# Optimization experiments

Measured on AMD Instinct MI355X. Metric: run time of the kernel, lower is better.

## Reference

```python
import jax, jax.numpy as jnp
import numpy as np
import math

B, S, D = 4, 1024, 1024
H, DK = 16, 64
NUM_BUCKETS, MAX_DIST = 32, 128


def _relative_position_bucket(relative_position, num_buckets=NUM_BUCKETS, max_distance=MAX_DIST):
    # bidirectional bucketing (T5 encoder style)
    num_buckets = num_buckets // 2
    buckets = (relative_position > 0).astype(jnp.int32) * num_buckets
    rp = jnp.abs(relative_position)
    max_exact = num_buckets // 2
    is_small = rp < max_exact
    # clamp to >=1 to avoid log(0); masked out by is_small anyway
    rp_large = max_exact + (
        jnp.log(jnp.maximum(rp, 1).astype(jnp.float32) / max_exact)
        / math.log(max_distance / max_exact)
        * (num_buckets - max_exact)
    ).astype(jnp.int32)
    rp_large = jnp.minimum(rp_large, num_buckets - 1)
    return buckets + jnp.where(is_small, rp, rp_large)


def compute_bias(rel_bias_table, q_len, k_len):
    ctx = jnp.arange(q_len)[:, None]
    mem = jnp.arange(k_len)[None, :]
    buckets = _relative_position_bucket(mem - ctx)  # [q,k]
    values = rel_bias_table[buckets]  # [q,k,H]
    return jnp.transpose(values, (2, 0, 1))  # [H,q,k]


def setup_inputs() -> dict:
    key = jax.random.key(0)
    ks = jax.random.split(key, 6)
    return {
        "hidden_states": jax.random.normal(ks[0], (B, S, D), dtype=jnp.float32),
        "Wq": jax.random.normal(ks[1], (D, H * DK), dtype=jnp.float32) * 0.02,
        "Wk": jax.random.normal(ks[2], (D, H * DK), dtype=jnp.float32) * 0.02,
        "Wv": jax.random.normal(ks[3], (D, H * DK), dtype=jnp.float32) * 0.02,
        "Wo": jax.random.normal(ks[4], (H * DK, D), dtype=jnp.float32) * 0.02,
        "rel_bias_table": jax.random.normal(ks[5], (NUM_BUCKETS, H), dtype=jnp.float32),
    }


def reference(hidden_states, Wq, Wk, Wv, Wo, rel_bias_table):
    b, s, _ = hidden_states.shape
    # projections (no bias), split heads -> [b,h,s,dk]
    def heads(x):
        return jnp.transpose(x.reshape(b, s, H, DK), (0, 2, 1, 3))
    q = heads(hidden_states @ Wq)
    k = heads(hidden_states @ Wk)
    v = heads(hidden_states @ Wv)
    # NOTE: T5 attention is UNSCALED (no 1/sqrt(dk))
    scores = jnp.einsum("bhqd,bhkd->bhqk", q, k)
    bias = compute_bias(rel_bias_table, s, s)[None]  # [1,H,s,s]
    scores = scores + bias
    attn = jax.nn.softmax(scores.astype(jnp.float32), axis=-1).astype(scores.dtype)
    out = jnp.einsum("bhqk,bhkd->bhqd", attn, v)
    out = jnp.transpose(out, (0, 2, 1, 3)).reshape(b, s, H * DK)
    return out @ Wo
```

## Files before the change

### kernel.cpp

```cpp
#include <hip/hip_runtime.h>
#include <hip/hip_bf16.h>

typedef __attribute__((ext_vector_type(8))) short short8;
typedef __attribute__((ext_vector_type(4))) float f32x4;
typedef __attribute__((ext_vector_type(4))) unsigned u32x4;
typedef unsigned short u16;

#define AS1 __attribute__((address_space(1)))
#define AS3 __attribute__((address_space(3)))

#define LOG2E 1.44269504088896f
#define FOLD_M 46.166241308446828f
#define EXP2(x) __builtin_amdgcn_exp2f(x)
#define WAITV(n) asm volatile("s_waitcnt vmcnt(" #n ")" ::: "memory")

__device__ __forceinline__ u16 f2bf(float f) {
    unsigned u = __builtin_bit_cast(unsigned, f);
    u += 0x7FFFu + ((u >> 16) & 1u);
    return (u16)(u >> 16);
}

__device__ __forceinline__ unsigned pk2(float a, float b) {
    unsigned ua = __builtin_bit_cast(unsigned, a) + 0x8000u;
    unsigned ub = __builtin_bit_cast(unsigned, b) + 0x8000u;
    return __builtin_amdgcn_perm(ub, ua, 0x07060302);
}

__global__ __launch_bounds__(256) void k_prep(const float* __restrict__ hidden,
                                              const float* __restrict__ Wq, const float* __restrict__ Wk,
                                              const float* __restrict__ Wv, const float* __restrict__ Wo,
                                              const float* __restrict__ tbl,
                                              u16* __restrict__ hidb,
                                              u16* __restrict__ wt, u16* __restrict__ wot,
                                              float* __restrict__ bias2) {
    int z = blockIdx.z;
    if (z >= 5) {
        int i = ((z - 5) * 1024 + blockIdx.y * 32 + blockIdx.x) * 256 + threadIdx.x;
        float4 v = ((const float4*)hidden)[i];
        ushort4 o;
        o.x = f2bf(v.x); o.y = f2bf(v.y); o.z = f2bf(v.z); o.w = f2bf(v.w);
        ((ushort4*)hidb)[i] = o;
        return;
    }
    if (z == 4) {
        int idx = (blockIdx.y * 32 + blockIdx.x) * 256 + threadIdx.x;
        if (idx < 16 * 2048) {
            int r = idx & 2047, h = idx >> 11;
            int rel = r - 1023;
            int bucket = rel > 0 ? 16 : 0;
            int rp = rel < 0 ? -rel : rel;
            if (rp < 8) bucket += rp;
            else {
                int lb = 8 + (int)(log2f((float)rp * 0.125f) * 2.0f);
                bucket += (lb < 15 ? lb : 15);
            }
            bias2[idx] = tbl[bucket * 16 + h] * LOG2E - FOLD_M;
        }
        return;
    }
    const float* in = z == 0 ? Wq : z == 1 ? Wk : z == 2 ? Wv : Wo;
    u16* out = (z == 3) ? wot : wt + (size_t)z * 1024 * 1024;
    __shared__ float tile[32][33];
    int tx = threadIdx.x & 31, ty = threadIdx.x >> 5;
    int bx = blockIdx.x << 5, by = blockIdx.y << 5;
    #pragma unroll
    for (int j = 0; j < 32; j += 8)
        tile[ty + j][tx] = in[(size_t)(by + ty + j) * 1024 + bx + tx];
    __syncthreads();
    #pragma unroll
    for (int j = 0; j < 32; j += 8)
        out[(size_t)(bx + ty + j) * 1024 + by + tx] = f2bf(tile[tx][ty + j]);
}

__global__ __launch_bounds__(512, 2) void k_qkv(const u16* __restrict__ A, const u16* __restrict__ Bt,
                                                u16* __restrict__ oq, u16* __restrict__ ok,
                                                u16* __restrict__ ov) {
    __shared__ __align__(16) u16 As[2][256 * 64];
    __shared__ __align__(16) u16 Bs[2][192 * 64];
    int t = threadIdx.x, lane = t & 63, wave = t >> 6;
    int g = lane >> 4, ln = lane & 15;
    int wr = wave >> 2, wc = wave & 3;

    int bid = blockIdx.x;
    int xcd = bid & 7, wgl = bid >> 3;
    int mt = ((xcd & 3) << 2) + (wgl >> 3);
    int nt = ((xcd >> 2) << 3) + (wgl & 7);
    int m0 = mt << 8, n0 = nt * 192;

    f32x4 acc[8][3];
    #pragma unroll
    for (int i = 0; i < 8; i++)
        #pragma unroll
        for (int j = 0; j < 3; j++) acc[i][j] = (f32x4){0.f, 0.f, 0.f, 0.f};

    #define QSTG(kt_, buf_)                                                                      \
        {                                                                                        \
            _Pragma("unroll")                                                                    \
            for (int u = 0; u < 4; u++) {                                                        \
                int L = t * 16 + u * 8192;                                                       \
                int row = L >> 7, gI = (L >> 4) & 7, gp = gI ^ (row & 7);                        \
                __builtin_amdgcn_global_load_lds(                                                \
                    (const AS1 void*)(A + (size_t)(m0 + row) * 1024 + (kt_) * 64 + gp * 8),      \
                    (AS3 void*)&As[buf_][L >> 1], 16, 0, 0);                                     \
            }                                                                                    \
            _Pragma("unroll")                                                                    \
            for (int u = 0; u < 3; u++) {                                                        \
                int L = t * 16 + u * 8192;                                                       \
                int row = L >> 7, gI = (L >> 4) & 7, gp = gI ^ (row & 7);                        \
                __builtin_amdgcn_global_load_lds(                                                \
                    (const AS1 void*)(Bt + (size_t)(n0 + row) * 1024 + (kt_) * 64 + gp * 8),     \
                    (AS3 void*)&Bs[buf_][L >> 1], 16, 0, 0);                                     \
            }                                                                                    \
        }

    QSTG(0, 0);
    __syncthreads();

    #pragma unroll 2
    for (int kt = 0; kt < 16; kt++) {
        const int c = kt & 1;
        if (kt < 15) QSTG(kt + 1, c ^ 1);

        #pragma unroll
        for (int ks = 0; ks < 2; ks++) {
            short8 af[8], bfr[3];
            int cb = ((ks << 2) + g) << 4;
            #pragma unroll
            for (int mf = 0; mf < 8; mf++) {
                int row = (wr << 7) + (mf << 4) + ln;
                af[mf] = *(const short8*)((const char*)&As[c][0] + row * 128 + (cb ^ ((row & 7) << 4)));
            }
            #pragma unroll
            for (int nf = 0; nf < 3; nf++) {
                int row = wc * 48 + (nf << 4) + ln;
                bfr[nf] = *(const short8*)((const char*)&Bs[c][0] + row * 128 + (cb ^ ((row & 7) << 4)));
            }
            __builtin_amdgcn_s_setprio(1);
            #pragma unroll
            for (int mf = 0; mf < 8; mf++)
                #pragma unroll
                for (int nf = 0; nf < 3; nf++)
                    acc[mf][nf] = __builtin_amdgcn_mfma_f32_16x16x32_bf16(af[mf], bfr[nf], acc[mf][nf], 0, 0, 0);
            __builtin_amdgcn_s_setprio(0);
        }
        __syncthreads();
    }
    #undef QSTG

    #pragma unroll
    for (int mf = 0; mf < 8; mf++)
        #pragma unroll
        for (int nf = 0; nf < 3; nf++) {
            int mb = m0 + (wr << 7) + (mf << 4) + (g << 2);
            int n = n0 + wc * 48 + (nf << 4) + ln;
            int j = n >> 10, col = n & 1023;
            int h = col >> 6, dk = col & 63;
            int b = mb >> 10, s = mb & 1023;
            if (j == 2) {
                ushort4 pk;
                pk.x = f2bf(acc[mf][nf][0]); pk.y = f2bf(acc[mf][nf][1]);
                pk.z = f2bf(acc[mf][nf][2]); pk.w = f2bf(acc[mf][nf][3]);
                *(ushort4*)(ov + ((size_t)(((b << 4) + h) * 64 + dk)) * 1024 + s) = pk;
            } else {
                u16* dst = (j == 0) ? oq : ok;
                #pragma unroll
                for (int r = 0; r < 4; r++)
                    dst[((size_t)(((b << 4) + h) * 1024 + s + r)) * 64 + dk] = f2bf(acc[mf][nf][r]);
            }
        }
}

__global__ __launch_bounds__(256) void k_gemm_out(const u16* __restrict__ A, const u16* __restrict__ Bt,
                                                  float* __restrict__ outf) {
    const int K = 1024, N = 1024;
    __shared__ __align__(16) u16 As[3][2048];
    __shared__ __align__(16) u16 Bs[3][4096];
    int t = threadIdx.x, lane = t & 63, wave = t >> 6;
    int bid = blockIdx.y * 8 + blockIdx.x;
    int sbid = (bid & 7) * 64 + (bid >> 3);
    int m0 = (sbid / 8) * 64, n0 = (sbid % 8) << 7;
    int wm = (wave >> 1) * 32, wn = (wave & 1) << 6;
    int g = lane >> 4, ln = lane & 15;
    f32x4 acc[2][4];
    #pragma unroll
    for (int i = 0; i < 2; i++)
        #pragma unroll
        for (int j = 0; j < 4; j++) acc[i][j] = (f32x4){0.f, 0.f, 0.f, 0.f};

    int schunk = ((lane & 3) ^ ((lane >> 3) & 3)) << 3;
    const u16* gA = A + (size_t)(m0 + wave * 16 + (lane >> 2)) * K + schunk;
    const u16* gB = Bt + (size_t)(n0 + wave * 16 + (lane >> 2)) * K + schunk;
    int ldsOff = wave * 512;

    #define GSTAGE(k0_, buf_)                                                                          \
        {                                                                                              \
            u16* sA = &As[buf_][0];                                                                    \
            u16* sB = &Bs[buf_][0];                                                                    \
            __builtin_amdgcn_global_load_lds((const AS1 void*)(gA + (k0_)),                            \
                                             (AS3 void*)&sA[ldsOff], 16, 0, 0);                        \
            __builtin_amdgcn_global_load_lds((const AS1 void*)(gB + (k0_)),                            \
                                             (AS3 void*)&sB[ldsOff], 16, 0, 0);                        \
            __builtin_amdgcn_global_load_lds((const AS1 void*)(gB + 64 * K + (k0_)),                   \
                                             (AS3 void*)&sB[ldsOff + 2048], 16, 0, 0);                 \
        }

    GSTAGE(0, 0);
    GSTAGE(32, 1);

    int rchunk = (g ^ ((ln >> 1) & 3)) << 3;
    int c0 = 0, c2 = 2;

    for (int kb = 0; kb < 32; kb++) {
        if (kb < 30) {
            GSTAGE((kb + 2) * 32, c2);
            WAITV(6);
        } else if (kb == 30) {
            WAITV(3);
        } else {
            WAITV(0);
        }
        __builtin_amdgcn_s_barrier();

        const u16* rA = &As[c0][0];
        const u16* rB = &Bs[c0][0];
        short8 af[2], bfr[4];
        #pragma unroll
        for (int fm = 0; fm < 2; fm++)
            af[fm] = *(const short8*)&rA[(wm + (fm << 4) + ln) * 32 + rchunk];
        #pragma unroll
        for (int fn = 0; fn < 4; fn++)
            bfr[fn] = *(const short8*)&rB[(wn + (fn << 4) + ln) * 32 + rchunk];
        __builtin_amdgcn_s_setprio(1);
        #pragma unroll
        for (int fm = 0; fm < 2; fm++)
            #pragma unroll
            for (int fn = 0; fn < 4; fn++)
                acc[fm][fn] = __builtin_amdgcn_mfma_f32_16x16x32_bf16(af[fm], bfr[fn], acc[fm][fn], 0, 0, 0);
        __builtin_amdgcn_s_setprio(0);
        __builtin_amdgcn_s_barrier();

        int old = c0;
        c0 = (c0 == 2) ? 0 : c0 + 1;
        c2 = old;
    }

    #pragma unroll
    for (int fm = 0; fm < 2; fm++)
        #pragma unroll
        for (int fn = 0; fn < 4; fn++) {
            int mb = m0 + wm + (fm << 4) + (g << 2);
            int n = n0 + wn + (fn << 4) + ln;
            #pragma unroll
            for (int r = 0; r < 4; r++)
                outf[(size_t)(mb + r) * N + n] = acc[fm][fn][r];
        }
    #undef GSTAGE
}

__global__ __launch_bounds__(256, 2) void k_attn(const u16* __restrict__ Qg, const u16* __restrict__ Kg,
                                                 const u16* __restrict__ Vtg, const float* __restrict__ bias2,
                                                 u16* __restrict__ attn_out) {
    __shared__ __align__(16) u16 Ks[2][64 * 64];
    __shared__ __align__(16) u16 Vts[2][64 * 64];
    __shared__ __align__(16) float blds4[4][1160];

    int t = threadIdx.x, lane = t & 63, w = t >> 6;
    int bid = blockIdx.x;
    int sid = (bid & 7) * 64 + (bid >> 3);
    int qb = sid & 7, h = (sid >> 3) & 15, b = sid >> 7;
    int q0 = qb << 7;
    const u16* Qh = Qg + ((size_t)(((b << 4) + h) * 1024 + q0)) * 64;
    const u16* Kh = Kg + (size_t)(((b << 4) + h)) * 1024 * 64;
    const u16* Vth = Vtg + (size_t)(((b << 4) + h)) * 64 * 1024;
    const float* bh = bias2 + (h << 11);

    int g = lane >> 4, ln = lane & 15;
    int lnk = (ln & 3) | ((ln & 4) << 1) | ((ln & 8) >> 1);
    int kbq = ((g & 1) << 3) | ((g >> 1) << 2);

    short8 qf[2][2];
    #pragma unroll
    for (int fm = 0; fm < 2; fm++)
        #pragma unroll
        for (int kh = 0; kh < 2; kh++)
            qf[fm][kh] = *(const short8*)(Qh + (size_t)(w * 32 + fm * 16 + ln) * 64 + kh * 32 + g * 8);

    int w0 = 896 - q0;
    for (int i = t; i < 1152; i += 256) {
        float v = bh[w0 + i];
        #pragma unroll
        for (int a2 = 0; a2 < 4; a2++) { int x = i - a2; if (x >= 0) blds4[a2][x] = v; }
    }
    float b_hi = bh[1023 + 256];
    float b_lo = bh[1023 - 256];
    int aRep = (3 - ln) & 3;
    const float* repB = &blds4[aRep][0];

    #define STAGE(kb_, buf_)                                                                     \
        {                                                                                        \
            _Pragma("unroll")                                                                    \
            for (int r2 = 0; r2 < 2; r2++) {                                                     \
                int L = t * 16 + r2 * 4096;                                                      \
                int row = L >> 7, gI = (L >> 4) & 7, gp = gI ^ (row & 7);                        \
                __builtin_amdgcn_global_load_lds(                                                \
                    (const AS1 void*)(Kh + (size_t)((kb_) * 64 + row) * 64 + gp * 8),            \
                    (AS3 void*)&Ks[buf_][L >> 1], 16, 0, 0);                                     \
                __builtin_amdgcn_global_load_lds(                                                \
                    (const AS1 void*)(Vth + (size_t)row * 1024 + (kb_) * 64 + gp * 8),           \
                    (AS3 void*)&Vts[buf_][L >> 1], 16, 0, 0);                                    \
            }                                                                                    \
        }

    STAGE(0, 0);
    __syncthreads();

    float psum[2] = {0.f, 0.f};
    f32x4 o[2][4];
    #pragma unroll
    for (int fm = 0; fm < 2; fm++)
        #pragma unroll
        for (int dn = 0; dn < 4; dn++) o[fm][dn] = (f32x4){0.f, 0.f, 0.f, 0.f};

    #pragma unroll 2
    for (int kb = 0; kb < 16; kb++) {
        const int cur = kb & 1;
        if (kb < 15) STAGE(kb + 1, cur ^ 1);

        f32x4 s[2][4];
        __builtin_amdgcn_s_setprio(1);
        #pragma unroll
        for (int fn = 0; fn < 4; fn++) {
            int row = (fn << 4) + lnk;
            short8 kf0 = *(const short8*)((const char*)Ks[cur] + row * 128 + (((g << 4) + 0)  ^ ((row & 7) << 4)));
            short8 kf1 = *(const short8*)((const char*)Ks[cur] + row * 128 + (((g << 4) + 64) ^ ((row & 7) << 4)));
            #pragma unroll
            for (int fm = 0; fm < 2; fm++) {
                f32x4 a = (f32x4){0.f, 0.f, 0.f, 0.f};
                a = __builtin_amdgcn_mfma_f32_16x16x32_bf16(kf0, qf[fm][0], a, 0, 0, 0);
                a = __builtin_amdgcn_mfma_f32_16x16x32_bf16(kf1, qf[fm][1], a, 0, 0, 0);
                s[fm][fn] = a;
            }
        }
        __builtin_amdgcn_s_setprio(0);

        int d0 = 64 * kb - q0 - 32 * w;
        int ibase = 64 * kb - 32 * w + 127 + kbq - ln;
        bool fast = (d0 >= 122) || (d0 <= -154);
        float bu = d0 > 0 ? b_hi : b_lo;
        unsigned Px[2][4], Py[2][4];
        #pragma unroll
        for (int fm = 0; fm < 2; fm++)
            #pragma unroll
            for (int fn = 0; fn < 4; fn++) {
                f32x4 sv = s[fm][fn];
                float b0, b1, b2v, b3;
                if (fast) { b0 = b1 = b2v = b3 = bu; }
                else {
                    float4 bb = *(const float4*)(repB + (ibase + 16 * fn - 16 * fm - aRep));
                    b0 = bb.x; b1 = bb.y; b2v = bb.z; b3 = bb.w;
                }
                float p0 = EXP2(fmaf(sv[0], LOG2E, b0));
                float p1 = EXP2(fmaf(sv[1], LOG2E, b1));
                float p2 = EXP2(fmaf(sv[2], LOG2E, b2v));
                float p3 = EXP2(fmaf(sv[3], LOG2E, b3));
                psum[fm] += (p0 + p1) + (p2 + p3);
                Px[fm][fn] = pk2(p0, p1);
                Py[fm][fn] = pk2(p2, p3);
            }

        short8 pa[2][2];
        #pragma unroll
        for (int fm = 0; fm < 2; fm++)
            #pragma unroll
            for (int ks = 0; ks < 2; ks++) {
                unsigned w0r = Px[fm][2 * ks], w2r = Px[fm][2 * ks + 1];
                unsigned w1r = Py[fm][2 * ks], w3r = Py[fm][2 * ks + 1];
                asm volatile("s_nop 1\n\tv_permlane32_swap_b32 %0, %1" : "+v"(w0r), "+v"(w2r));
                asm volatile("s_nop 1\n\tv_permlane32_swap_b32 %0, %1" : "+v"(w1r), "+v"(w3r));
                u32x4 tv; tv[0] = w0r; tv[1] = w1r; tv[2] = w2r; tv[3] = w3r;
                pa[fm][ks] = __builtin_bit_cast(short8, tv);
            }

        __builtin_amdgcn_s_setprio(1);
        #pragma unroll
        for (int dn = 0; dn < 4; dn++) {
            int vrow = (dn << 4) + ln;
            short8 vb0 = *(const short8*)((const char*)Vts[cur] + vrow * 128 + (((g << 4) + 0)  ^ ((vrow & 7) << 4)));
            short8 vb1 = *(const short8*)((const char*)Vts[cur] + vrow * 128 + (((g << 4) + 64) ^ ((vrow & 7) << 4)));
            #pragma unroll
            for (int fm = 0; fm < 2; fm++) {
                f32x4 a = o[fm][dn];
                a = __builtin_amdgcn_mfma_f32_16x16x32_bf16(pa[fm][0], vb0, a, 0, 0, 0);
                a = __builtin_amdgcn_mfma_f32_16x16x32_bf16(pa[fm][1], vb1, a, 0, 0, 0);
                o[fm][dn] = a;
            }
        }
        __builtin_amdgcn_s_setprio(0);

        __syncthreads();
    }

    float linv[2][4];
    #pragma unroll
    for (int fm = 0; fm < 2; fm++) {
        float v = psum[fm];
        v += __shfl_xor(v, 16);
        v += __shfl_xor(v, 32);
        float inv = 1.0f / v;
        #pragma unroll
        for (int r = 0; r < 4; r++)
            linv[fm][r] = __shfl(inv, 4 * g + r);
    }
    #pragma unroll
    for (int fm = 0; fm < 2; fm++)
        #pragma unroll
        for (int dn = 0; dn < 4; dn++)
            #pragma unroll
            for (int r = 0; r < 4; r++) {
                int srow = q0 + 32 * w + 16 * fm + (g << 2) + r;
                int col = (h << 6) + (dn << 4) + ln;
                attn_out[((size_t)((b << 10) + srow) << 10) + col] = f2bf(o[fm][dn][r] * linv[fm][r]);
            }
}

extern "C" void kernel_launch(void* const* d_in, const int* in_sizes, int n_in,
                              void* d_out, int out_size, void* d_ws, size_t ws_size,
                              hipStream_t stream) {
    const float* hidden = (const float*)d_in[0];
    const float* Wq = (const float*)d_in[1];
    const float* Wk = (const float*)d_in[2];
    const float* Wv = (const float*)d_in[3];
    const float* Wo = (const float*)d_in[4];
    const float* tbl = (const float*)d_in[5];

    u16* hidb = (u16*)d_ws;
    u16* wt   = hidb + 4096 * 1024;
    u16* wot  = wt + 3072 * 1024;
    u16* Qb   = wot + 1024 * 1024;
    u16* Kb   = Qb + 4 * 16 * 1024 * 64;
    u16* Vb   = Kb + 4 * 16 * 1024 * 64;
    u16* attn = Vb + 4 * 16 * 1024 * 64;
    float* bias = (float*)(attn + 4096 * 1024);

    k_prep<<<dim3(32, 32, 9), 256, 0, stream>>>(hidden, Wq, Wk, Wv, Wo, tbl, hidb, wt, wot, bias);
    k_qkv<<<256, 512, 0, stream>>>(hidb, wt, Qb, Kb, Vb);
    k_attn<<<512, 256, 0, stream>>>(Qb, Kb, Vb, bias, attn);
    k_gemm_out<<<dim3(8, 64), 256, 0, stream>>>(attn, wot, (float*)d_out);
}
```

Measured before the change: 95.88 us.

## Fuse hidden-state bf16 conversion into QKV GEMM and retile output GEMM

The separate fp32-to-bf16 pass over hidden_states in the prep kernel is removed. The QKV GEMM now loads fp32 A tiles into registers, converts them and writes them to LDS after the MFMA step, which overlaps that load with compute and saves one global write and read of the activation. The output GEMM moves from 64x128 tiles with a 3-stage buffer and manual vmcnt waits to 128x128 tiles with a 2-stage buffer and __syncthreads, halving the grid. setprio hints are also dropped. Costs are extra register pressure in k_qkv, doubled fp32 A traffic per tile load, and lower occupancy and less latency hiding in the output GEMM.

```diff
diff --git a/kernel.cpp b/kernel.cpp
--- a/kernel.cpp
+++ b/kernel.cpp
@@ -12,7 +12,6 @@
 #define LOG2E 1.44269504088896f
 #define FOLD_M 46.166241308446828f
 #define EXP2(x) __builtin_amdgcn_exp2f(x)
-#define WAITV(n) asm volatile("s_waitcnt vmcnt(" #n ")" ::: "memory")
 
 __device__ __forceinline__ u16 f2bf(float f) {
     unsigned u = __builtin_bit_cast(unsigned, f);
@@ -20,28 +19,22 @@
     return (u16)(u >> 16);
 }
 
+__device__ __forceinline__ unsigned pkrne(float a, float b) {
+    return (unsigned)f2bf(a) | ((unsigned)f2bf(b) << 16);
+}
+
 __device__ __forceinline__ unsigned pk2(float a, float b) {
     unsigned ua = __builtin_bit_cast(unsigned, a) + 0x8000u;
     unsigned ub = __builtin_bit_cast(unsigned, b) + 0x8000u;
     return __builtin_amdgcn_perm(ub, ua, 0x07060302);
 }
 
-__global__ __launch_bounds__(256) void k_prep(const float* __restrict__ hidden,
-                                              const float* __restrict__ Wq, const float* __restrict__ Wk,
+__global__ __launch_bounds__(256) void k_prep(const float* __restrict__ Wq, const float* __restrict__ Wk,
                                               const float* __restrict__ Wv, const float* __restrict__ Wo,
                                               const float* __restrict__ tbl,
-                                              u16* __restrict__ hidb,
                                               u16* __restrict__ wt, u16* __restrict__ wot,
                                               float* __restrict__ bias2) {
     int z = blockIdx.z;
-    if (z >= 5) {
-        int i = ((z - 5) * 1024 + blockIdx.y * 32 + blockIdx.x) * 256 + threadIdx.x;
-        float4 v = ((const float4*)hidden)[i];
-        ushort4 o;
-        o.x = f2bf(v.x); o.y = f2bf(v.y); o.z = f2bf(v.z); o.w = f2bf(v.w);
-        ((ushort4*)hidb)[i] = o;
-        return;
-    }
     if (z == 4) {
         int idx = (blockIdx.y * 32 + blockIdx.x) * 256 + threadIdx.x;
         if (idx < 16 * 2048) {
@@ -72,7 +65,7 @@
         out[(size_t)(bx + ty + j) * 1024 + by + tx] = f2bf(tile[tx][ty + j]);
 }
 
-__global__ __launch_bounds__(512, 2) void k_qkv(const u16* __restrict__ A, const u16* __restrict__ Bt,
+__global__ __launch_bounds__(512, 2) void k_qkv(const float* __restrict__ A32, const u16* __restrict__ Bt,
                                                 u16* __restrict__ oq, u16* __restrict__ ok,
                                                 u16* __restrict__ ov) {
     __shared__ __align__(16) u16 As[2][256 * 64];
@@ -87,22 +80,16 @@
     int nt = ((xcd >> 2) << 3) + (wgl & 7);
     int m0 = mt << 8, n0 = nt * 192;
 
+    int arow = t >> 1, akh = t & 1;
+
     f32x4 acc[8][3];
     #pragma unroll
     for (int i = 0; i < 8; i++)
         #pragma unroll
         for (int j = 0; j < 3; j++) acc[i][j] = (f32x4){0.f, 0.f, 0.f, 0.f};
 
-    #define QSTG(kt_, buf_)                                                                      \
+    #define QSTG_B(kt_, buf_)                                                                    \
         {                                                                                        \
-            _Pragma("unroll")                                                                    \
-            for (int u = 0; u < 4; u++) {                                                        \
-                int L = t * 16 + u * 8192;                                                       \
-                int row = L >> 7, gI = (L >> 4) & 7, gp = gI ^ (row & 7);                        \
-                __builtin_amdgcn_global_load_lds(                                                \
-                    (const AS1 void*)(A + (size_t)(m0 + row) * 1024 + (kt_) * 64 + gp * 8),      \
-                    (AS3 void*)&As[buf_][L >> 1], 16, 0, 0);                                     \
-            }                                                                                    \
             _Pragma("unroll")                                                                    \
             for (int u = 0; u < 3; u++) {                                                        \
                 int L = t * 16 + u * 8192;                                                       \
@@ -113,13 +100,42 @@
             }                                                                                    \
         }
 
-    QSTG(0, 0);
+    #define ALOAD(kt_, av_)                                                                      \
+        {                                                                                        \
+            const float4* s4 = (const float4*)(A32 + (size_t)(m0 + arow) * 1024 + (kt_) * 64 + akh * 32); \
+            _Pragma("unroll")                                                                    \
+            for (int j = 0; j < 8; j++) av_[j] = s4[j];                                          \
+        }
+
+    #define AWRITE(av_, buf_)                                                                    \
+        {                                                                                        \
+            _Pragma("unroll")                                                                    \
+            for (int j = 0; j < 4; j++) {                                                        \
+                u32x4 wv;                                                                        \
+                wv[0] = pkrne(av_[2 * j].x, av_[2 * j].y);                                       \
+                wv[1] = pkrne(av_[2 * j].z, av_[2 * j].w);                                       \
+                wv[2] = pkrne(av_[2 * j + 1].x, av_[2 * j + 1].y);                               \
+                wv[3] = pkrne(av_[2 * j + 1].z, av_[2 * j + 1].w);                               \
+                *(u32x4*)((char*)&As[buf_][0] + arow * 128 + ((((akh << 2) + j) ^ (arow & 7)) << 4)) = wv; \
+            }                                                                                    \
+        }
+
+    {
+        float4 av0[8];
+        ALOAD(0, av0);
+        QSTG_B(0, 0);
+        AWRITE(av0, 0);
+    }
     __syncthreads();
 
     #pragma unroll 2
     for (int kt = 0; kt < 16; kt++) {
         const int c = kt & 1;
-        if (kt < 15) QSTG(kt + 1, c ^ 1);
+        float4 av[8];
+        if (kt < 15) {
+            ALOAD(kt + 1, av);
+            QSTG_B(kt + 1, c ^ 1);
+        }
 
         #pragma unroll
         for (int ks = 0; ks < 2; ks++) {
@@ -135,17 +151,20 @@
                 int row = wc * 48 + (nf << 4) + ln;
                 bfr[nf] = *(const short8*)((const char*)&Bs[c][0] + row * 128 + (cb ^ ((row & 7) << 4)));
             }
-            __builtin_amdgcn_s_setprio(1);
             #pragma unroll
             for (int mf = 0; mf < 8; mf++)
                 #pragma unroll
                 for (int nf = 0; nf < 3; nf++)
                     acc[mf][nf] = __builtin_amdgcn_mfma_f32_16x16x32_bf16(af[mf], bfr[nf], acc[mf][nf], 0, 0, 0);
-            __builtin_amdgcn_s_setprio(0);
-        }
+        }
+
+        if (kt < 15) AWRITE(av, c ^ 1);
+
         __syncthreads();
     }
-    #undef QSTG
+    #undef QSTG_B
+    #undef ALOAD
+    #undef AWRITE
 
     #pragma unroll
     for (int mf = 0; mf < 8; mf++)
@@ -173,17 +192,17 @@
 __global__ __launch_bounds__(256) void k_gemm_out(const u16* __restrict__ A, const u16* __restrict__ Bt,
                                                   float* __restrict__ outf) {
     const int K = 1024, N = 1024;
-    __shared__ __align__(16) u16 As[3][2048];
-    __shared__ __align__(16) u16 Bs[3][4096];
+    __shared__ __align__(16) u16 As[2][8192];
+    __shared__ __align__(16) u16 Bs[2][8192];
     int t = threadIdx.x, lane = t & 63, wave = t >> 6;
     int bid = blockIdx.y * 8 + blockIdx.x;
-    int sbid = (bid & 7) * 64 + (bid >> 3);
-    int m0 = (sbid / 8) * 64, n0 = (sbid % 8) << 7;
-    int wm = (wave >> 1) * 32, wn = (wave & 1) << 6;
+    int sbid = (bid & 7) * 32 + (bid >> 3);
+    int m0 = (sbid >> 3) << 7, n0 = (sbid & 7) << 7;
+    int wm = (wave >> 1) << 6, wn = (wave & 1) << 6;
     int g = lane >> 4, ln = lane & 15;
-    f32x4 acc[2][4];
-    #pragma unroll
-    for (int i = 0; i < 2; i++)
+    f32x4 acc[4][4];
+    #pragma unroll
+    for (int i = 0; i < 4; i++)
         #pragma unroll
         for (int j = 0; j < 4; j++) acc[i][j] = (f32x4){0.f, 0.f, 0.f, 0.f};
 
@@ -194,58 +213,44 @@
 
     #define GSTAGE(k0_, buf_)                                                                          \
         {                                                                                              \
-            u16* sA = &As[buf_][0];                                                                    \
-            u16* sB = &Bs[buf_][0];                                                                    \
             __builtin_amdgcn_global_load_lds((const AS1 void*)(gA + (k0_)),                            \
-                                             (AS3 void*)&sA[ldsOff], 16, 0, 0);                        \
+                                             (AS3 void*)&As[buf_][ldsOff], 16, 0, 0);                  \
+            __builtin_amdgcn_global_load_lds((const AS1 void*)(gA + 64 * K + (k0_)),                   \
+                                             (AS3 void*)&As[buf_][ldsOff + 2048], 16, 0, 0);           \
             __builtin_amdgcn_global_load_lds((const AS1 void*)(gB + (k0_)),                            \
-                                             (AS3 void*)&sB[ldsOff], 16, 0, 0);                        \
+                                             (AS3 void*)&Bs[buf_][ldsOff], 16, 0, 0);                  \
             __builtin_amdgcn_global_load_lds((const AS1 void*)(gB + 64 * K + (k0_)),                   \
-                                             (AS3 void*)&sB[ldsOff + 2048], 16, 0, 0);                 \
+                                             (AS3 void*)&Bs[buf_][ldsOff + 2048], 16, 0, 0);           \
         }
 
     GSTAGE(0, 0);
-    GSTAGE(32, 1);
+    __syncthreads();
 
     int rchunk = (g ^ ((ln >> 1) & 3)) << 3;
-    int c0 = 0, c2 = 2;
-
+
+    #pragma unroll 2
     for (int kb = 0; kb < 32; kb++) {
-        if (kb < 30) {
-            GSTAGE((kb + 2) * 32, c2);
-            WAITV(6);
-        } else if (kb == 30) {
-            WAITV(3);
-        } else {
-            WAITV(0);
-        }
-        __builtin_amdgcn_s_barrier();
-
-        const u16* rA = &As[c0][0];
-        const u16* rB = &Bs[c0][0];
-        short8 af[2], bfr[4];
-        #pragma unroll
-        for (int fm = 0; fm < 2; fm++)
-            af[fm] = *(const short8*)&rA[(wm + (fm << 4) + ln) * 32 + rchunk];
+        const int cur = kb & 1;
+        if (kb < 31) GSTAGE((kb + 1) * 32, cur ^ 1);
+
+        short8 af[4], bfr[4];
+        #pragma unroll
+        for (int fm = 0; fm < 4; fm++)
+            af[fm] = *(const short8*)&As[cur][(wm + (fm << 4) + ln) * 32 + rchunk];
         #pragma unroll
         for (int fn = 0; fn < 4; fn++)
-            bfr[fn] = *(const short8*)&rB[(wn + (fn << 4) + ln) * 32 + rchunk];
-        __builtin_amdgcn_s_setprio(1);
-        #pragma unroll
-        for (int fm = 0; fm < 2; fm++)
+            bfr[fn] = *(const short8*)&Bs[cur][(wn + (fn << 4) + ln) * 32 + rchunk];
+        #pragma unroll
+        for (int fm = 0; fm < 4; fm++)
             #pragma unroll
             for (int fn = 0; fn < 4; fn++)
                 acc[fm][fn] = __builtin_amdgcn_mfma_f32_16x16x32_bf16(af[fm], bfr[fn], acc[fm][fn], 0, 0, 0);
-        __builtin_amdgcn_s_setprio(0);
-        __builtin_amdgcn_s_barrier();
-
-        int old = c0;
-        c0 = (c0 == 2) ? 0 : c0 + 1;
-        c2 = old;
-    }
-
-    #pragma unroll
-    for (int fm = 0; fm < 2; fm++)
+
+        __syncthreads();
+    }
+
+    #pragma unroll
+    for (int fm = 0; fm < 4; fm++)
         #pragma unroll
         for (int fn = 0; fn < 4; fn++) {
             int mb = m0 + wm + (fm << 4) + (g << 2);
@@ -433,8 +438,7 @@
     const float* Wo = (const float*)d_in[4];
     const float* tbl = (const float*)d_in[5];
 
-    u16* hidb = (u16*)d_ws;
-    u16* wt   = hidb + 4096 * 1024;
+    u16* wt   = (u16*)d_ws;
     u16* wot  = wt + 3072 * 1024;
     u16* Qb   = wot + 1024 * 1024;
     u16* Kb   = Qb + 4 * 16 * 1024 * 64;
@@ -442,8 +446,8 @@
     u16* attn = Vb + 4 * 16 * 1024 * 64;
     float* bias = (float*)(attn + 4096 * 1024);
 
-    k_prep<<<dim3(32, 32, 9), 256, 0, stream>>>(hidden, Wq, Wk, Wv, Wo, tbl, hidb, wt, wot, bias);
-    k_qkv<<<256, 512, 0, stream>>>(hidb, wt, Qb, Kb, Vb);
+    k_prep<<<dim3(32, 32, 5), 256, 0, stream>>>(Wq, Wk, Wv, Wo, tbl, wt, wot, bias);
+    k_qkv<<<256, 512, 0, stream>>>(hidden, wt, Qb, Kb, Vb);
     k_attn<<<512, 256, 0, stream>>>(Qb, Kb, Vb, bias, attn);
-    k_gemm_out<<<dim3(8, 64), 256, 0, stream>>>(attn, wot, (float*)d_out);
-}
+    k_gemm_out<<<dim3(8, 32), 256, 0, stream>>>(attn, wot, (float*)d_out);
+}
```

New measurement: 118.7 us. +23.8%, slower.

## Enlarge output GEMM tile to 128x128 with simple double-buffered loop

Applied to the files above, without the earlier changes.

The output projection GEMM moves from 64x128 block tiles to 128x128 tiles, giving each wave a 64x64 sub-tile with a 4x4 MFMA accumulator grid. This raises data reuse per LDS load. The three-stage pipeline with explicit vmcnt waits and setprio is replaced by a two-stage double buffer synchronized with __syncthreads, and the grid is halved to 256 blocks. In exchange, the kernel runs with fewer waves per CU, shallower prefetch and more accumulator registers, which can reduce latency hiding.

```diff
diff --git a/kernel.cpp b/kernel.cpp
--- a/kernel.cpp
+++ b/kernel.cpp
@@ -12,7 +12,6 @@
 #define LOG2E 1.44269504088896f
 #define FOLD_M 46.166241308446828f
 #define EXP2(x) __builtin_amdgcn_exp2f(x)
-#define WAITV(n) asm volatile("s_waitcnt vmcnt(" #n ")" ::: "memory")
 
 __device__ __forceinline__ u16 f2bf(float f) {
     unsigned u = __builtin_bit_cast(unsigned, f);
@@ -173,17 +172,17 @@
 __global__ __launch_bounds__(256) void k_gemm_out(const u16* __restrict__ A, const u16* __restrict__ Bt,
                                                   float* __restrict__ outf) {
     const int K = 1024, N = 1024;
-    __shared__ __align__(16) u16 As[3][2048];
-    __shared__ __align__(16) u16 Bs[3][4096];
+    __shared__ __align__(16) u16 As[2][8192];
+    __shared__ __align__(16) u16 Bs[2][8192];
     int t = threadIdx.x, lane = t & 63, wave = t >> 6;
     int bid = blockIdx.y * 8 + blockIdx.x;
-    int sbid = (bid & 7) * 64 + (bid >> 3);
-    int m0 = (sbid / 8) * 64, n0 = (sbid % 8) << 7;
-    int wm = (wave >> 1) * 32, wn = (wave & 1) << 6;
+    int sbid = (bid & 7) * 32 + (bid >> 3);
+    int m0 = (sbid >> 3) << 7, n0 = (sbid & 7) << 7;
+    int wm = (wave >> 1) << 6, wn = (wave & 1) << 6;
     int g = lane >> 4, ln = lane & 15;
-    f32x4 acc[2][4];
-    #pragma unroll
-    for (int i = 0; i < 2; i++)
+    f32x4 acc[4][4];
+    #pragma unroll
+    for (int i = 0; i < 4; i++)
         #pragma unroll
         for (int j = 0; j < 4; j++) acc[i][j] = (f32x4){0.f, 0.f, 0.f, 0.f};
 
@@ -194,58 +193,44 @@
 
     #define GSTAGE(k0_, buf_)                                                                          \
         {                                                                                              \
-            u16* sA = &As[buf_][0];                                                                    \
-            u16* sB = &Bs[buf_][0];                                                                    \
             __builtin_amdgcn_global_load_lds((const AS1 void*)(gA + (k0_)),                            \
-                                             (AS3 void*)&sA[ldsOff], 16, 0, 0);                        \
+                                             (AS3 void*)&As[buf_][ldsOff], 16, 0, 0);                  \
+            __builtin_amdgcn_global_load_lds((const AS1 void*)(gA + 64 * K + (k0_)),                   \
+                                             (AS3 void*)&As[buf_][ldsOff + 2048], 16, 0, 0);           \
             __builtin_amdgcn_global_load_lds((const AS1 void*)(gB + (k0_)),                            \
-                                             (AS3 void*)&sB[ldsOff], 16, 0, 0);                        \
+                                             (AS3 void*)&Bs[buf_][ldsOff], 16, 0, 0);                  \
             __builtin_amdgcn_global_load_lds((const AS1 void*)(gB + 64 * K + (k0_)),                   \
-                                             (AS3 void*)&sB[ldsOff + 2048], 16, 0, 0);                 \
+                                             (AS3 void*)&Bs[buf_][ldsOff + 2048], 16, 0, 0);           \
         }
 
     GSTAGE(0, 0);
-    GSTAGE(32, 1);
+    __syncthreads();
 
     int rchunk = (g ^ ((ln >> 1) & 3)) << 3;
-    int c0 = 0, c2 = 2;
-
+
+    #pragma unroll 2
     for (int kb = 0; kb < 32; kb++) {
-        if (kb < 30) {
-            GSTAGE((kb + 2) * 32, c2);
-            WAITV(6);
-        } else if (kb == 30) {
-            WAITV(3);
-        } else {
-            WAITV(0);
-        }
-        __builtin_amdgcn_s_barrier();
-
-        const u16* rA = &As[c0][0];
-        const u16* rB = &Bs[c0][0];
-        short8 af[2], bfr[4];
-        #pragma unroll
-        for (int fm = 0; fm < 2; fm++)
-            af[fm] = *(const short8*)&rA[(wm + (fm << 4) + ln) * 32 + rchunk];
+        const int cur = kb & 1;
+        if (kb < 31) GSTAGE((kb + 1) * 32, cur ^ 1);
+
+        short8 af[4], bfr[4];
+        #pragma unroll
+        for (int fm = 0; fm < 4; fm++)
+            af[fm] = *(const short8*)&As[cur][(wm + (fm << 4) + ln) * 32 + rchunk];
         #pragma unroll
         for (int fn = 0; fn < 4; fn++)
-            bfr[fn] = *(const short8*)&rB[(wn + (fn << 4) + ln) * 32 + rchunk];
-        __builtin_amdgcn_s_setprio(1);
-        #pragma unroll
-        for (int fm = 0; fm < 2; fm++)
+            bfr[fn] = *(const short8*)&Bs[cur][(wn + (fn << 4) + ln) * 32 + rchunk];
+        #pragma unroll
+        for (int fm = 0; fm < 4; fm++)
             #pragma unroll
             for (int fn = 0; fn < 4; fn++)
                 acc[fm][fn] = __builtin_amdgcn_mfma_f32_16x16x32_bf16(af[fm], bfr[fn], acc[fm][fn], 0, 0, 0);
-        __builtin_amdgcn_s_setprio(0);
-        __builtin_amdgcn_s_barrier();
-
-        int old = c0;
-        c0 = (c0 == 2) ? 0 : c0 + 1;
-        c2 = old;
-    }
-
-    #pragma unroll
-    for (int fm = 0; fm < 2; fm++)
+
+        __syncthreads();
+    }
+
+    #pragma unroll
+    for (int fm = 0; fm < 4; fm++)
         #pragma unroll
         for (int fn = 0; fn < 4; fn++) {
             int mb = m0 + wm + (fm << 4) + (g << 2);
@@ -445,5 +430,5 @@
     k_prep<<<dim3(32, 32, 9), 256, 0, stream>>>(hidden, Wq, Wk, Wv, Wo, tbl, hidb, wt, wot, bias);
     k_qkv<<<256, 512, 0, stream>>>(hidb, wt, Qb, Kb, Vb);
     k_attn<<<512, 256, 0, stream>>>(Qb, Kb, Vb, bias, attn);
-    k_gemm_out<<<dim3(8, 64), 256, 0, stream>>>(attn, wot, (float*)d_out);
-}
+    k_gemm_out<<<dim3(8, 32), 256, 0, stream>>>(attn, wot, (float*)d_out);
+}
```

Measured after the change: 97.10 us. No clear change (+1.3%).
